# Performance work log

Measured on AMD Instinct MI355X. Metric: run time of the kernel, lower is better.

Reference implementation:

```python
import jax, jax.numpy as jnp
import numpy as np
from jax import lax

B, T, D, H = 4096, 256, 18, 32


def setup_inputs() -> dict:
    key = jax.random.key(0)
    ks = jax.random.split(key, 9)
    s = 1.0 / np.sqrt(H)  # PyTorch LSTM init scale
    return {
        "batch": jax.random.normal(ks[0], (B, T, D), dtype=jnp.float32),
        "W_ih": jax.random.normal(ks[1], (4 * H, D), dtype=jnp.float32) * s,
        "W_hh": jax.random.normal(ks[2], (4 * H, H), dtype=jnp.float32) * s,
        "b_ih": jax.random.normal(ks[3], (4 * H,), dtype=jnp.float32) * s,
        "b_hh": jax.random.normal(ks[4], (4 * H,), dtype=jnp.float32) * s,
        "W1": jax.random.normal(ks[5], (512, H * T), dtype=jnp.float32) * 0.02,
        "b1": jax.random.normal(ks[6], (512,), dtype=jnp.float32) * 0.02,
        "W2": jax.random.normal(ks[7], (1, 512), dtype=jnp.float32) * 0.02,
        "b2": jax.random.normal(ks[8], (1,), dtype=jnp.float32) * 0.02,
    }


def _lstm(batch, W_ih, W_hh, b_ih, b_hh):
    b, t, _ = batch.shape
    h = batch.dtype.type
    # Precompute input projections for all timesteps: [B, T, 4H]
    x_proj = jnp.einsum('bti,gi->btg', batch, W_ih) + b_ih + b_hh
    W_hh_T = W_hh.T  # [H, 4H]

    def step(carry, xp):
        h_prev, c_prev = carry
        gates = xp + h_prev @ W_hh_T  # [B, 4H]
        i, f, g, o = jnp.split(gates, 4, axis=-1)  # PyTorch gate order i,f,g,o
        i = jax.nn.sigmoid(i)
        f = jax.nn.sigmoid(f)
        g = jnp.tanh(g)
        o = jax.nn.sigmoid(o)
        c = f * c_prev + i * g
        h_new = o * jnp.tanh(c)
        return (h_new, c), h_new

    h0 = jnp.zeros((b, H), dtype=batch.dtype)
    c0 = jnp.zeros((b, H), dtype=batch.dtype)
    _, hs = lax.scan(step, (h0, c0), x_proj.transpose(1, 0, 2))  # hs: [T, B, H]
    return hs.transpose(1, 0, 2)  # [B, T, H]


def reference(batch, W_ih, W_hh, b_ih, b_hh, W1, b1, W2, b2):
    hs = _lstm(batch, W_ih, W_hh, b_ih, b_hh)            # [B, T, H]
    flat = hs.reshape(hs.shape[0], -1)                   # [B, T*H]
    hid = jax.nn.relu(flat @ W1.T + b1)                  # [B, 512]
    return hid @ W2.T + b2                               # [B, 1]
```

## Files before the change

kernel.cpp:

```cpp
#include <hip/hip_runtime.h>
#include <hip/hip_bf16.h>
#include <stdint.h>

typedef float f32x4 __attribute__((ext_vector_type(4)));
typedef _Float16 half8 __attribute__((ext_vector_type(8)));

#define B_ 4096
#define T_ 256
#define D_ 18
#define H_ 32
#define GK 8192
#define GN 512
#define KSPLIT 4
#define SLOT 520

#define K1_ 1.442695041f
#define K2_ 2.885390082f
#define X2_ __builtin_amdgcn_exp2f
#define RCP_ __builtin_amdgcn_rcpf

__device__ __forceinline__ void ldsbar() {
  asm volatile("s_waitcnt lgkmcnt(0)\n\ts_barrier" ::: "memory");
}
__device__ __forceinline__ void gl_lds16(const _Float16* g, _Float16* l) {
  __builtin_amdgcn_global_load_lds(
      (const __attribute__((address_space(1))) unsigned int*)g,
      (__attribute__((address_space(3))) unsigned int*)l, 16, 0, 0);
}

__global__ __launch_bounds__(256) void cvtw1_kernel(const float* __restrict__ w1,
                                                    unsigned short* __restrict__ dst) {
  int i = blockIdx.x * 256 + threadIdx.x;
  float4 v = ((const float4*)w1)[i];
  unsigned short a = __builtin_bit_cast(unsigned short, (_Float16)v.x);
  unsigned short b = __builtin_bit_cast(unsigned short, (_Float16)v.y);
  unsigned short c = __builtin_bit_cast(unsigned short, (_Float16)v.z);
  unsigned short d = __builtin_bit_cast(unsigned short, (_Float16)v.w);
  uint2 o; o.x = (unsigned)a | ((unsigned)b << 16); o.y = (unsigned)c | ((unsigned)d << 16);
  ((uint2*)dst)[i] = o;
}

__global__ __launch_bounds__(512) void lstm_kernel(
    const float* __restrict__ batch, const float* __restrict__ W_ih,
    const float* __restrict__ W_hh, const float* __restrict__ b_ih,
    const float* __restrict__ b_hh, _Float16* __restrict__ hs) {
  __shared__ _Float16 hist[16 * SLOT];
  __shared__ _Float16 xs[2 * 4096];

  const int tid = (int)threadIdx.x;
  const int lane = tid & 63;
  const int w = tid >> 6;
  const int lq = lane >> 4;
  const int lr = lane & 15;
  const int b0 = (int)blockIdx.x * 16;

  half8 wx, wh;
  {
    int grow = (lr & 3) * 32 + w * 4 + (lr >> 2);
#pragma unroll
    for (int j = 0; j < 8; ++j) {
      int k = lq * 8 + j;
      wx[j] = (k < D_) ? (_Float16)W_ih[grow * D_ + k] : (_Float16)0.0f;
      wh[j] = (_Float16)W_hh[grow * H_ + k];
    }
  }
  f32x4 bias4;
#pragma unroll
  for (int r = 0; r < 4; ++r) {
    int g = r * 32 + w * 4 + lq;
    bias4[r] = b_ih[g] + b_hh[g];
  }

  const int rdo = lr * 32 + ((lq ^ ((lr >> 1) & 3)) << 3);
  const int kcol = w * 4 + lq;
  const int wro = lr * 32 + ((((kcol >> 3) ^ ((lr >> 1) & 3))) << 3) + (kcol & 7);

  const int fe = tid >> 5;
  const int fs = (tid >> 2) & 7;
  const int fg = tid & 3;
  const int fl_rd = fs * SLOT + fe * 32 + ((fg ^ ((fe >> 1) & 3)) << 3);
  _Float16* fl_wp = hs + (size_t)(b0 + fe) * GK + fs * H_ + fg * 8;

  const int e0 = tid / 36, q0 = tid - e0 * 36;
  const int i1 = tid + 512;
  const int e1 = i1 / 36, q1 = i1 - e1 * 36;
  const float* xld0 = batch + (size_t)(b0 + e0) * (T_ * D_) + q0 * 4;
  const float* xld1 = batch + (size_t)(b0 + e1) * (T_ * D_) + q1 * 4;
  float4 xv0, xv1;

#define XLOAD(tb)                                                              \
  do {                                                                         \
    xv0 = *(const float4*)(xld0 + (tb) * 144);                                 \
    if (tid < 64) xv1 = *(const float4*)(xld1 + (tb) * 144);                   \
  } while (0)

#define XPUT(E, Q, V, buf)                                                     \
  do {                                                                         \
    int swz_ = ((E) >> 1) & 3;                                                 \
    _Pragma("unroll") for (int j = 0; j < 4; ++j) {                            \
      int f_ = (Q) * 4 + j;                                                    \
      int to_ = (f_ * 57) >> 10;                          \
      int d_ = f_ - to_ * 18;                                                  \
      float val_ = (j == 0) ? (V).x : (j == 1) ? (V).y : (j == 2) ? (V).z : (V).w; \
      xs[(buf) * 4096 + to_ * 512 + (E) * 32 + (((d_ >> 3) ^ swz_) << 3) + (d_ & 7)] = \
          (_Float16)val_;                                                      \
    }                                                                          \
  } while (0)

#define XSTORE(buf)                                                            \
  do {                                                                         \
    XPUT(e0, q0, xv0, buf);                                                    \
    if (tid < 64) XPUT(e1, q1, xv1, buf);                                      \
  } while (0)

#define STEP(tt, AXC, PRE)                                                     \
  do {                                                                         \
    _Float16* hrd = ((tt) == 0 ? po + 7 * SLOT : pr + ((tt)-1) * SLOT);        \
    half8 hf = *(const half8*)&hrd[rdo];                                       \
    f32x4 acc = __builtin_amdgcn_mfma_f32_16x16x32_f16(wh, hf, AXC, 0, 0, 0);  \
    PRE;                                                                       \
    float ei = X2_(-K1_ * acc[0]);                                             \
    float ef = X2_(-K1_ * acc[1]);                                             \
    float eg = X2_(-K2_ * acc[2]);                                             \
    float eo = X2_(-K1_ * acc[3]);                                             \
    float pi_ = (1.0f + ei) * (1.0f + eg);                                     \
    float num = fmaf(c, pi_, (1.0f + ef) * (1.0f - eg));                       \
    c = num * RCP_((1.0f + ef) * pi_);                                         \
    float ec = X2_(-K2_ * c);                                                  \
    float h = (1.0f - ec) * RCP_((1.0f + eo) * (1.0f + ec));                   \
    pr[(tt)*SLOT + wro] = (_Float16)h;                                         \
    ldsbar();                                                                  \
  } while (0)

  XLOAD(0);
  for (int i = tid; i < 16 * SLOT; i += 512) hist[i] = (_Float16)0.0f;
  for (int i = tid; i < 8192; i += 512) xs[i] = (_Float16)0.0f;
  ldsbar();
  XSTORE(0);
  XLOAD(1);
  ldsbar();

  float c = 0.0f;
  for (int blk = 0; blk < 32; ++blk) {
    const int p = blk & 1;
    _Float16* pr = hist + p * (8 * SLOT);
    _Float16* po = hist + (p ^ 1) * (8 * SLOT);
    const int xo = p * 4096;

    half8 xq[8];
#pragma unroll
    for (int j = 0; j < 8; ++j) xq[j] = *(const half8*)&xs[xo + j * 512 + rdo];
    f32x4 ax0, ax1;
    ax0 = __builtin_amdgcn_mfma_f32_16x16x32_f16(wx, xq[0], bias4, 0, 0, 0);

    STEP(0, ax0, ax1 = __builtin_amdgcn_mfma_f32_16x16x32_f16(wx, xq[1], bias4, 0, 0, 0));
    STEP(1, ax1, ax0 = __builtin_amdgcn_mfma_f32_16x16x32_f16(wx, xq[2], bias4, 0, 0, 0));
    STEP(2, ax0, ax1 = __builtin_amdgcn_mfma_f32_16x16x32_f16(wx, xq[3], bias4, 0, 0, 0));
    STEP(3, ax1, ax0 = __builtin_amdgcn_mfma_f32_16x16x32_f16(wx, xq[4], bias4, 0, 0, 0));
    if (blk < 31) XSTORE(p ^ 1);
    if (blk < 30) XLOAD(blk + 2);
    STEP(4, ax0, ax1 = __builtin_amdgcn_mfma_f32_16x16x32_f16(wx, xq[5], bias4, 0, 0, 0));
    if (blk) {
      half8 hv = *(const half8*)&hist[(p ^ 1) * (8 * SLOT) + fl_rd];
      *(half8*)(fl_wp + (size_t)(blk - 1) * (8 * H_)) = hv;
    }
    STEP(5, ax1, ax0 = __builtin_amdgcn_mfma_f32_16x16x32_f16(wx, xq[6], bias4, 0, 0, 0));
    STEP(6, ax0, ax1 = __builtin_amdgcn_mfma_f32_16x16x32_f16(wx, xq[7], bias4, 0, 0, 0));
    STEP(7, ax1, );
  }
  {
    half8 hv = *(const half8*)&hist[8 * SLOT + fl_rd];
    *(half8*)(fl_wp + (size_t)31 * (8 * H_)) = hv;
  }
#undef STEP
#undef XSTORE
#undef XPUT
#undef XLOAD
}

__global__ __launch_bounds__(256, 2) void gemm_kernel(
    const _Float16* __restrict__ Ahs, const _Float16* __restrict__ Bw1,
    _Float16* __restrict__ part) {
  __shared__ _Float16 As[2 * 128 * 64];
  __shared__ _Float16 Bs[2 * 128 * 64];

  const int bid = (int)blockIdx.x;
  const int m0 = (bid & 31) << 7;
  const int n0 = ((bid >> 5) & 3) << 7;
  const int ksp = bid >> 7;
  const int k0 = ksp << 11;
  _Float16* outp = part + (size_t)ksp * ((size_t)B_ * GN);

  const int tid = (int)threadIdx.x;
  const int lane = tid & 63, w = tid >> 6;
  const int wm = w & 1, wn = w >> 1;
  const int lq = lane >> 4, lr = lane & 15;

  const _Float16* gA[4]; const _Float16* gB[4];
  _Float16* lA[4]; _Float16* lB[4];
#pragma unroll
  for (int j = 0; j < 4; ++j) {
    int p = tid + 256 * j;
    int row = p >> 3, q = p & 7, cg = q ^ (row & 7);
    gA[j] = Ahs + (size_t)(m0 + row) * GK + k0 + cg * 8;
    gB[j] = Bw1 + (size_t)(n0 + row) * GK + k0 + cg * 8;
    int wbase = (w * 64 + 256 * j) * 8;
    lA[j] = As + wbase;
    lB[j] = Bs + wbase;
  }

  int offA[4][2], offB[4][2];
#pragma unroll
  for (int mt = 0; mt < 4; ++mt)
#pragma unroll
    for (int ks = 0; ks < 2; ++ks) {
      int m = wm * 64 + mt * 16 + lr;
      offA[mt][ks] = m * 64 + (((lq + ks * 4) ^ (m & 7)) << 3);
      int n = wn * 64 + mt * 16 + lr;
      offB[mt][ks] = n * 64 + (((lq + ks * 4) ^ (n & 7)) << 3);
    }

  f32x4 acc[4][4];
#pragma unroll
  for (int mt = 0; mt < 4; ++mt)
#pragma unroll
    for (int nt = 0; nt < 4; ++nt) {
      acc[mt][nt][0] = 0.f; acc[mt][nt][1] = 0.f;
      acc[mt][nt][2] = 0.f; acc[mt][nt][3] = 0.f;
    }

#define STAGE(POFF)                                                            \
  do {                                                                         \
    _Pragma("unroll") for (int j = 0; j < 4; ++j) {                            \
      gl_lds16(gA[j], lA[j] + (POFF));                                         \
      gl_lds16(gB[j], lB[j] + (POFF));                                         \
      gA[j] += 64; gB[j] += 64;                                                \
    }                                                                          \
  } while (0)

#define FRAGS(POFF)                                                            \
  half8 af[4][2], bf[4][2];                                                    \
  _Pragma("unroll") for (int mt = 0; mt < 4; ++mt)                             \
    _Pragma("unroll") for (int ks = 0; ks < 2; ++ks) {                         \
      af[mt][ks] = *(const half8*)&As[(POFF) + offA[mt][ks]];                  \
      bf[mt][ks] = *(const half8*)&Bs[(POFF) + offB[mt][ks]];                  \
    }

#define MFMAS                                                                  \
  _Pragma("unroll") for (int ks = 0; ks < 2; ++ks)                             \
    _Pragma("unroll") for (int mt = 0; mt < 4; ++mt)                           \
      _Pragma("unroll") for (int nt = 0; nt < 4; ++nt)                         \
        acc[mt][nt] = __builtin_amdgcn_mfma_f32_16x16x32_f16(                  \
            af[mt][ks], bf[nt][ks], acc[mt][nt], 0, 0, 0);

  STAGE(0);
  STAGE(8192);

  for (int it = 0; it < 31; ++it) {
    const int POFF = (it & 1) * 8192;
    asm volatile("s_waitcnt vmcnt(8)\n\ts_barrier" ::: "memory");
    FRAGS(POFF);
    asm volatile("s_waitcnt lgkmcnt(0)\n\ts_barrier" ::: "memory");
    if (it < 30) STAGE(POFF);
    MFMAS;
  }
  {
    asm volatile("s_waitcnt vmcnt(0)\n\ts_barrier" ::: "memory");
    FRAGS(8192);
    MFMAS;
  }
#undef MFMAS
#undef FRAGS
#undef STAGE

#pragma unroll
  for (int mt = 0; mt < 4; ++mt)
#pragma unroll
    for (int nt = 0; nt < 4; ++nt) {
      int n = n0 + wn * 64 + nt * 16 + lr;
#pragma unroll
      for (int r = 0; r < 4; ++r) {
        int m = m0 + wm * 64 + mt * 16 + lq * 4 + r;
        outp[(size_t)m * GN + n] = (_Float16)acc[mt][nt][r];
      }
    }
}

__global__ __launch_bounds__(256) void head_kernel(const _Float16* __restrict__ part,
                                                   const float* __restrict__ b1,
                                                   const float* __restrict__ W2,
                                                   const float* __restrict__ b2,
                                                   float* __restrict__ out) {
  const int b = (int)(blockIdx.x * 4 + (threadIdx.x >> 6));
  const int l = (int)(threadIdx.x & 63);
  const size_t stride = (size_t)B_ * GN;
  half8 hv = ((const half8*)(part + (size_t)b * GN))[l];
  float a8[8];
#pragma unroll
  for (int j = 0; j < 8; ++j) a8[j] = (float)hv[j];
#pragma unroll
  for (int sp = 1; sp < KSPLIT; ++sp) {
    half8 pv = ((const half8*)(part + sp * stride + (size_t)b * GN))[l];
#pragma unroll
    for (int j = 0; j < 8; ++j) a8[j] += (float)pv[j];
  }
  float4 bv0 = ((const float4*)b1)[2 * l];
  float4 bv1 = ((const float4*)b1)[2 * l + 1];
  float4 wv0 = ((const float4*)W2)[2 * l];
  float4 wv1 = ((const float4*)W2)[2 * l + 1];
  float s = 0.0f;
  s = fmaf(fmaxf(a8[0] + bv0.x, 0.0f), wv0.x, s);
  s = fmaf(fmaxf(a8[1] + bv0.y, 0.0f), wv0.y, s);
  s = fmaf(fmaxf(a8[2] + bv0.z, 0.0f), wv0.z, s);
  s = fmaf(fmaxf(a8[3] + bv0.w, 0.0f), wv0.w, s);
  s = fmaf(fmaxf(a8[4] + bv1.x, 0.0f), wv1.x, s);
  s = fmaf(fmaxf(a8[5] + bv1.y, 0.0f), wv1.y, s);
  s = fmaf(fmaxf(a8[6] + bv1.z, 0.0f), wv1.z, s);
  s = fmaf(fmaxf(a8[7] + bv1.w, 0.0f), wv1.w, s);
#pragma unroll
  for (int off = 32; off >= 1; off >>= 1) s += __shfl_xor(s, off);
  if (l == 0) out[b] = s + b2[0];
}

extern "C" void kernel_launch(void* const* d_in, const int* in_sizes, int n_in,
                              void* d_out, int out_size, void* d_ws, size_t ws_size,
                              hipStream_t stream) {
  const float* batch = (const float*)d_in[0];
  const float* W_ih = (const float*)d_in[1];
  const float* W_hh = (const float*)d_in[2];
  const float* b_ih = (const float*)d_in[3];
  const float* b_hh = (const float*)d_in[4];
  const float* W1 = (const float*)d_in[5];
  const float* b1 = (const float*)d_in[6];
  const float* W2 = (const float*)d_in[7];
  const float* b2 = (const float*)d_in[8];
  float* out = (float*)d_out;

  char* ws = (char*)d_ws;
  _Float16* hs = (_Float16*)ws;
  _Float16* w1h = (_Float16*)(ws + 67108864);
  _Float16* part = (_Float16*)(ws + 67108864 + 8388608);

  cvtw1_kernel<<<4096, 256, 0, stream>>>(W1, (unsigned short*)w1h);
  lstm_kernel<<<256, 512, 0, stream>>>(batch, W_ih, W_hh, b_ih, b_hh, hs);
  gemm_kernel<<<512, 256, 0, stream>>>(hs, w1h, part);
  head_kernel<<<1024, 256, 0, stream>>>(part, b1, W2, b2, out);
}
```

Before: 230.5 us.

## Use 256x256 GEMM tiles with eight-wave phased ping-pong pipeline

Restructures the fp16 MFMA GEMM to one 512-thread block per 256x256 output tile, doubling the K-split to 8 so 256 blocks still cover the device. Each K-step is split into eight phases that each issue a quarter of the next tile's global-to-LDS loads and then run a group of MFMAs, with raised wave priority during the MFMAs. The intent is to reuse each loaded tile across more output and overlap loads with compute more finely. In exchange it uses much more LDS and registers and leaves one block per CU. The larger K-split also doubles the partial-sum buffer that the head kernel must write and reduce.

Measured after the change: 230.1 us. Within noise of the previous version (-0.2%).

```diff
diff --git a/kernel.cpp b/kernel.cpp
--- a/kernel.cpp
+++ b/kernel.cpp
@@ -11,7 +11,7 @@
 #define H_ 32
 #define GK 8192
 #define GN 512
-#define KSPLIT 4
+#define KSPLIT 8
 #define SLOT 520
 
 #define K1_ 1.442695041f
@@ -178,109 +178,120 @@
 #undef XLOAD
 }
 
-__global__ __launch_bounds__(256, 2) void gemm_kernel(
+__global__ __launch_bounds__(512, 1) void gemm_kernel(
     const _Float16* __restrict__ Ahs, const _Float16* __restrict__ Bw1,
     _Float16* __restrict__ part) {
-  __shared__ _Float16 As[2 * 128 * 64];
-  __shared__ _Float16 Bs[2 * 128 * 64];
+  __shared__ _Float16 As[2 * 256 * 64];
+  __shared__ _Float16 Bs[2 * 256 * 64];
 
   const int bid = (int)blockIdx.x;
-  const int m0 = (bid & 31) << 7;
-  const int n0 = ((bid >> 5) & 3) << 7;
-  const int ksp = bid >> 7;
-  const int k0 = ksp << 11;
+  const int m0 = (bid & 15) << 8;
+  const int n0 = ((bid >> 4) & 1) << 8;
+  const int ksp = bid >> 5;
+  const int k0 = ksp << 10;
   _Float16* outp = part + (size_t)ksp * ((size_t)B_ * GN);
 
   const int tid = (int)threadIdx.x;
   const int lane = tid & 63, w = tid >> 6;
-  const int wm = w & 1, wn = w >> 1;
+  const int wm = w >> 2, wn = w & 3;
   const int lq = lane >> 4, lr = lane & 15;
 
   const _Float16* gA[4]; const _Float16* gB[4];
-  _Float16* lA[4]; _Float16* lB[4];
+  _Float16* lAd[4]; _Float16* lBd[4];
 #pragma unroll
   for (int j = 0; j < 4; ++j) {
-    int p = tid + 256 * j;
+    int p = tid + 512 * j;
     int row = p >> 3, q = p & 7, cg = q ^ (row & 7);
     gA[j] = Ahs + (size_t)(m0 + row) * GK + k0 + cg * 8;
     gB[j] = Bw1 + (size_t)(n0 + row) * GK + k0 + cg * 8;
-    int wbase = (w * 64 + 256 * j) * 8;
-    lA[j] = As + wbase;
-    lB[j] = Bs + wbase;
-  }
-
-  int offA[4][2], offB[4][2];
-#pragma unroll
-  for (int mt = 0; mt < 4; ++mt)
-#pragma unroll
-    for (int ks = 0; ks < 2; ++ks) {
-      int m = wm * 64 + mt * 16 + lr;
-      offA[mt][ks] = m * 64 + (((lq + ks * 4) ^ (m & 7)) << 3);
-      int n = wn * 64 + mt * 16 + lr;
-      offB[mt][ks] = n * 64 + (((lq + ks * 4) ^ (n & 7)) << 3);
-    }
-
-  f32x4 acc[4][4];
-#pragma unroll
-  for (int mt = 0; mt < 4; ++mt)
+    lAd[j] = As + (w * 64 + 512 * j) * 8;
+    lBd[j] = Bs + (w * 64 + 512 * j) * 8;
+  }
+
+  const int rA = (wm * 128 + lr) * 64;
+  const int rB = (wn * 64 + lr) * 64;
+  int xk[2];
+  xk[0] = ((lq) ^ (lr & 7)) << 3;
+  xk[1] = ((lq + 4) ^ (lr & 7)) << 3;
+
+  f32x4 acc[8][4];
+#pragma unroll
+  for (int mt = 0; mt < 8; ++mt)
 #pragma unroll
     for (int nt = 0; nt < 4; ++nt) {
       acc[mt][nt][0] = 0.f; acc[mt][nt][1] = 0.f;
       acc[mt][nt][2] = 0.f; acc[mt][nt][3] = 0.f;
     }
 
-#define STAGE(POFF)                                                            \
-  do {                                                                         \
-    _Pragma("unroll") for (int j = 0; j < 4; ++j) {                            \
-      gl_lds16(gA[j], lA[j] + (POFF));                                         \
-      gl_lds16(gB[j], lB[j] + (POFF));                                         \
-      gA[j] += 64; gB[j] += 64;                                                \
-    }                                                                          \
-  } while (0)
-
-#define FRAGS(POFF)                                                            \
-  half8 af[4][2], bf[4][2];                                                    \
-  _Pragma("unroll") for (int mt = 0; mt < 4; ++mt)                             \
-    _Pragma("unroll") for (int ks = 0; ks < 2; ++ks) {                         \
-      af[mt][ks] = *(const half8*)&As[(POFF) + offA[mt][ks]];                  \
-      bf[mt][ks] = *(const half8*)&Bs[(POFF) + offB[mt][ks]];                  \
-    }
-
-#define MFMAS                                                                  \
-  _Pragma("unroll") for (int ks = 0; ks < 2; ++ks)                             \
+#define SA2(J0, J1, SBUF, T)                                                   \
+  do {                                                                         \
+    gl_lds16(gA[J0] + (size_t)(T) * 64, lAd[J0] + (SBUF) * 16384);             \
+    gl_lds16(gA[J1] + (size_t)(T) * 64, lAd[J1] + (SBUF) * 16384);             \
+  } while (0)
+#define SB2(J0, J1, SBUF, T)                                                   \
+  do {                                                                         \
+    gl_lds16(gB[J0] + (size_t)(T) * 64, lBd[J0] + (SBUF) * 16384);             \
+    gl_lds16(gB[J1] + (size_t)(T) * 64, lBd[J1] + (SBUF) * 16384);             \
+  } while (0)
+
+#define PHASE(RBUF, MH, NH, STAGECODE, TAILWAIT)                               \
+  do {                                                                         \
+    half8 af[4][2], bf[2][2];                                                  \
     _Pragma("unroll") for (int mt = 0; mt < 4; ++mt)                           \
-      _Pragma("unroll") for (int nt = 0; nt < 4; ++nt)                         \
-        acc[mt][nt] = __builtin_amdgcn_mfma_f32_16x16x32_f16(                  \
-            af[mt][ks], bf[nt][ks], acc[mt][nt], 0, 0, 0);
-
-  STAGE(0);
-  STAGE(8192);
-
-  for (int it = 0; it < 31; ++it) {
-    const int POFF = (it & 1) * 8192;
-    asm volatile("s_waitcnt vmcnt(8)\n\ts_barrier" ::: "memory");
-    FRAGS(POFF);
-    asm volatile("s_waitcnt lgkmcnt(0)\n\ts_barrier" ::: "memory");
-    if (it < 30) STAGE(POFF);
-    MFMAS;
-  }
-  {
-    asm volatile("s_waitcnt vmcnt(0)\n\ts_barrier" ::: "memory");
-    FRAGS(8192);
-    MFMAS;
-  }
-#undef MFMAS
-#undef FRAGS
-#undef STAGE
-
-#pragma unroll
-  for (int mt = 0; mt < 4; ++mt)
+      _Pragma("unroll") for (int ks = 0; ks < 2; ++ks)                         \
+        af[mt][ks] = *(const half8*)&As[(RBUF) * 16384 + rA +                  \
+                                        ((MH) * 64 + mt * 16) * 64 + xk[ks]];  \
+    _Pragma("unroll") for (int nt = 0; nt < 2; ++nt)                           \
+      _Pragma("unroll") for (int ks = 0; ks < 2; ++ks)                         \
+        bf[nt][ks] = *(const half8*)&Bs[(RBUF) * 16384 + rB +                  \
+                                        ((NH) * 32 + nt * 16) * 64 + xk[ks]];  \
+    STAGECODE;                                                                 \
+    asm volatile("s_barrier" ::: "memory");                                    \
+    __builtin_amdgcn_s_setprio(1);                                             \
+    _Pragma("unroll") for (int ks = 0; ks < 2; ++ks)                           \
+      _Pragma("unroll") for (int mt = 0; mt < 4; ++mt)                         \
+        _Pragma("unroll") for (int nt = 0; nt < 2; ++nt)                       \
+          acc[(MH) * 4 + mt][(NH) * 2 + nt] =                                  \
+              __builtin_amdgcn_mfma_f32_16x16x32_f16(                          \
+                  af[mt][ks], bf[nt][ks], acc[(MH) * 4 + mt][(NH) * 2 + nt],   \
+                  0, 0, 0);                                                    \
+    __builtin_amdgcn_s_setprio(0);                                             \
+    TAILWAIT;                                                                  \
+    asm volatile("s_barrier" ::: "memory");                                    \
+  } while (0)
+
+#define VM0 asm volatile("s_waitcnt vmcnt(0)" ::: "memory")
+
+  SA2(0, 1, 0, 0); SA2(2, 3, 0, 0);
+  SB2(0, 1, 0, 0); SB2(2, 3, 0, 0);
+  asm volatile("s_waitcnt vmcnt(0)\n\ts_barrier" ::: "memory");
+
+  for (int it = 0; it < 8; ++it) {
+    const int t1 = 2 * it + 1;
+    const int t2 = 2 * it + 2;
+    const bool g2 = (t2 < 16);
+    PHASE(0, 0, 0, SA2(0, 1, 1, t1), );
+    PHASE(0, 0, 1, SA2(2, 3, 1, t1), );
+    PHASE(0, 1, 0, SB2(0, 1, 1, t1), );
+    PHASE(0, 1, 1, SB2(2, 3, 1, t1), VM0);
+    PHASE(1, 0, 0, if (g2) SA2(0, 1, 0, t2), );
+    PHASE(1, 0, 1, if (g2) SA2(2, 3, 0, t2), );
+    PHASE(1, 1, 0, if (g2) SB2(0, 1, 0, t2), );
+    PHASE(1, 1, 1, if (g2) SB2(2, 3, 0, t2), VM0);
+  }
+#undef VM0
+#undef PHASE
+#undef SB2
+#undef SA2
+
+#pragma unroll
+  for (int mt = 0; mt < 8; ++mt)
 #pragma unroll
     for (int nt = 0; nt < 4; ++nt) {
       int n = n0 + wn * 64 + nt * 16 + lr;
 #pragma unroll
       for (int r = 0; r < 4; ++r) {
-        int m = m0 + wm * 64 + mt * 16 + lq * 4 + r;
+        int m = m0 + wm * 128 + mt * 16 + lq * 4 + r;
         outp[(size_t)m * GN + n] = (_Float16)acc[mt][nt][r];
       }
     }
@@ -343,6 +354,6 @@
 
   cvtw1_kernel<<<4096, 256, 0, stream>>>(W1, (unsigned short*)w1h);
   lstm_kernel<<<256, 512, 0, stream>>>(batch, W_ih, W_hh, b_ih, b_hh, hs);
-  gemm_kernel<<<512, 256, 0, stream>>>(hs, w1h, part);
+  gemm_kernel<<<256, 512, 0, stream>>>(hs, w1h, part);
   head_kernel<<<1024, 256, 0, stream>>>(part, b1, W2, b2, out);
 }
```
